# Optimization experiments

Measured on AMD Instinct MI355X. Metric: run time of the kernel, lower is better.

## Reference

```python
import jax, jax.numpy as jnp
import numpy as np

IM_FE_RATIO = 16.0


def setup_inputs() -> dict:
    key = jax.random.key(0)
    k1, k2 = jax.random.split(key)
    B, C, H, W, N = 4, 128, 256, 256, 4096
    feature = jax.random.normal(k1, (B, C, H, W), dtype=jnp.float32)
    # keypoints in image-pixel coords, in range [0, (W-1)*im_fe_ratio]
    keypoints = jax.random.uniform(k2, (B, N, 2), dtype=jnp.float32,
                                   minval=0.0, maxval=(W - 1) * IM_FE_RATIO)
    return {"feature": feature, "keypoints": keypoints}


def _interpolate(feature, keypoints):
    B, C, H, W = feature.shape
    kp = keypoints / IM_FE_RATIO  # B x N x 2 in feature-map coords (x, y)
    max_xy = jnp.array([W - 1, H - 1], dtype=kp.dtype)
    lo = jnp.maximum(jnp.floor(kp), 0.0)   # B x N x 2
    hi = jnp.minimum(jnp.ceil(kp), max_xy)  # B x N x 2
    up = kp - lo                            # fractional part (weight for upper corner)
    lw = 1.0 - up                           # weight for lower corner

    # corner order matches torch code: (x0,y0), (x1,y0), (x0,y1), (x1,y1)
    ix = jnp.stack([lo[..., 0], hi[..., 0], lo[..., 0], hi[..., 0]], axis=-1).astype(jnp.int32)  # B x N x 4
    iy = jnp.stack([lo[..., 1], lo[..., 1], hi[..., 1], hi[..., 1]], axis=-1).astype(jnp.int32)  # B x N x 4
    wx = jnp.stack([lw[..., 0], up[..., 0], lw[..., 0], up[..., 0]], axis=-1)
    wy = jnp.stack([lw[..., 1], lw[..., 1], up[..., 1], up[..., 1]], axis=-1)
    coeff = wx * wy                          # B x N x 4

    idx = (iy * W + ix)                      # B x N x 4 flat spatial indices
    feat_flat = feature.reshape(B, C, H * W)

    # gather per batch: (C, HW)[:, (N,4)] -> C x N x 4
    gathered = jax.vmap(lambda f, i: f[:, i])(feat_flat, idx)  # B x C x N x 4
    uf = jnp.einsum('bcnk,bnk->bcn', gathered, coeff)          # B x C x N

    # mask off keypoints that are (0, 0): mean over the 2 coords of (kp > 1e-10)
    mask = (kp > 1e-10).astype(uf.dtype).mean(axis=2)          # B x N
    return uf * mask[:, None, :]


def reference(feature, keypoints):
    return _interpolate(feature, keypoints)
```

## Files before the change

kernel.cpp:

```cpp
#include <hip/hip_runtime.h>

#define BB 4
#define CC 128
#define HH 256
#define WW 256
#define NKP 4096
#define INV_RATIO (1.0f / 16.0f)
#define CPT 4
#define NXCD 8

typedef float fpair __attribute__((ext_vector_type(2)));

__global__ __launch_bounds__(256) void interp_kernel(
    const float* __restrict__ feature,
    const float* __restrict__ keypoints,
    float* __restrict__ out)
{
    int bid   = blockIdx.x;
    int xcd   = bid & (NXCD - 1);
    int slot  = bid >> 3;
    int gloc  = slot >> 4;
    int j     = slot & 15;
    int g     = gloc * NXCD + xcd;
    int b     = g >> 5;
    int c0    = (g & 31) * CPT;
    int n     = j * 256 + threadIdx.x;

    const float* kp = keypoints + ((size_t)(b * NKP + n)) * 2;
    float kx = kp[0] * INV_RATIO;
    float ky = kp[1] * INV_RATIO;

    float fx = fmaxf(floorf(kx), 0.0f);
    float fy = fmaxf(floorf(ky), 0.0f);
    int x0 = (int)fx, y0 = (int)fy;

    float ux = kx - fx, uy = ky - fy;
    float lx = 1.0f - ux, ly = 1.0f - uy;

    bool selx = (x0 >= WW - 1);
    bool sely = (y0 >= HH - 1);
    int xp = selx ? (WW - 2) : x0;
    int yp = sely ? (HH - 2) : y0;
    float wlx = selx ? 0.0f : lx, wux = selx ? 1.0f : ux;
    float wly = sely ? 0.0f : ly, wuy = sely ? 1.0f : uy;

    float mask = 0.5f * ((kx > 1e-10f ? 1.0f : 0.0f) + (ky > 1e-10f ? 1.0f : 0.0f));
    float w00 = wlx * wly * mask, w01 = wux * wly * mask;
    float w10 = wlx * wuy * mask, w11 = wux * wuy * mask;

    int i0 = yp * WW + xp;
    int i1 = i0 + WW;

    const float* f = feature + ((size_t)(b * CC + c0)) * (HH * WW);

    fpair r0[CPT], r1[CPT];
    #pragma unroll
    for (int k = 0; k < CPT; ++k) {
        const float* fc = f + (size_t)k * (HH * WW);
        __builtin_memcpy(&r0[k], fc + i0, sizeof(fpair));
        __builtin_memcpy(&r1[k], fc + i1, sizeof(fpair));
    }

    float* o = out + ((size_t)(b * CC + c0)) * NKP + n;
    #pragma unroll
    for (int k = 0; k < CPT; ++k) {
        float val = w00 * r0[k].x + w01 * r0[k].y
                  + w10 * r1[k].x + w11 * r1[k].y;
        __builtin_nontemporal_store(val, o + (size_t)k * NKP);
    }
}

extern "C" void kernel_launch(void* const* d_in, const int* in_sizes, int n_in,
                              void* d_out, int out_size, void* d_ws, size_t ws_size,
                              hipStream_t stream) {
    const float* feature   = (const float*)d_in[0];
    const float* keypoints = (const float*)d_in[1];
    float* out = (float*)d_out;

    const int grid = BB * (CC / CPT) * (NKP / 256);
    interp_kernel<<<grid, 256, 0, stream>>>(feature, keypoints, out);
}
```

Measured before the change: 30.39 us.

## Counting-sort keypoints by spatial bin before gathering, then permute results back

```diff
diff --git a/kernel.cpp b/kernel.cpp
--- a/kernel.cpp
+++ b/kernel.cpp
@@ -11,7 +11,150 @@
 
 typedef float fpair __attribute__((ext_vector_type(2)));
 
-__global__ __launch_bounds__(256) void interp_kernel(
+#define O_INV  (BB * NKP * 2 * 4)
+#define O_VS   (256 * 1024)
+#define WS_NEEDED (O_VS + (size_t)BB * CC * NKP * 4)
+
+__global__ __launch_bounds__(1024) void sort_kernel(
+    const float* __restrict__ keypoints,
+    float* __restrict__ sorted_kp,
+    unsigned* __restrict__ inv)
+{
+    __shared__ unsigned bins[4096];
+    __shared__ unsigned wtot[16];
+    __shared__ unsigned wexc[16];
+    const int b = blockIdx.x;
+    const int t = threadIdx.x;
+    const int lane = t & 63, wid = t >> 6;
+
+    #pragma unroll
+    for (int k = 0; k < 4; ++k) bins[t + 1024 * k] = 0u;
+    __syncthreads();
+
+    unsigned key[4];
+    float kxv[4], kyv[4];
+    #pragma unroll
+    for (int k = 0; k < 4; ++k) {
+        int n = t + 1024 * k;
+        const float* kp = keypoints + ((size_t)(b * NKP + n)) * 2;
+        float kx = kp[0] * INV_RATIO, ky = kp[1] * INV_RATIO;
+        kxv[k] = kx; kyv[k] = ky;
+        int x0 = (int)fmaxf(floorf(kx), 0.0f);
+        int y0 = (int)fmaxf(floorf(ky), 0.0f);
+        unsigned bin = ((unsigned)y0 << 4) | ((unsigned)x0 >> 4);
+        key[k] = bin;
+        atomicAdd(&bins[bin], 1u);
+    }
+    __syncthreads();
+
+    unsigned c0 = bins[4*t], c1 = bins[4*t+1], c2 = bins[4*t+2], c3 = bins[4*t+3];
+    unsigned s = c0 + c1 + c2 + c3;
+    unsigned v = s;
+    #pragma unroll
+    for (int d = 1; d < 64; d <<= 1) {
+        unsigned u = __shfl_up(v, d, 64);
+        if (lane >= d) v += u;
+    }
+    if (lane == 63) wtot[wid] = v;
+    __syncthreads();
+    if (t == 0) { unsigned acc = 0; for (int w = 0; w < 16; ++w) { wexc[w] = acc; acc += wtot[w]; } }
+    __syncthreads();
+    unsigned texc = wexc[wid] + (v - s);
+    bins[4*t]   = texc;
+    bins[4*t+1] = texc + c0;
+    bins[4*t+2] = texc + c0 + c1;
+    bins[4*t+3] = texc + c0 + c1 + c2;
+    __syncthreads();
+
+    #pragma unroll
+    for (int k = 0; k < 4; ++k) {
+        int n = t + 1024 * k;
+        unsigned pos = atomicAdd(&bins[key[k]], 1u);
+        float* dst = sorted_kp + ((size_t)(b * NKP) + pos) * 2;
+        dst[0] = kxv[k];
+        dst[1] = kyv[k];
+        inv[b * NKP + n] = pos;
+    }
+}
+
+__global__ __launch_bounds__(256) void gather_kernel(
+    const float* __restrict__ feature,
+    const float* __restrict__ sorted_kp,
+    float* __restrict__ out_sorted)
+{
+    int bid   = blockIdx.x;
+    int xcd   = bid & (NXCD - 1);
+    int slot  = bid >> 3;
+    int gloc  = slot >> 4;
+    int j     = slot & 15;
+    int g     = gloc * NXCD + xcd;
+    int b     = g >> 5;
+    int c0    = (g & 31) * CPT;
+    int i     = j * 256 + threadIdx.x;
+
+    fpair kpv;
+    __builtin_memcpy(&kpv, sorted_kp + ((size_t)(b * NKP) + i) * 2, sizeof(fpair));
+    float kx = kpv.x, ky = kpv.y;
+
+    float fx = fmaxf(floorf(kx), 0.0f);
+    float fy = fmaxf(floorf(ky), 0.0f);
+    int x0 = (int)fx, y0 = (int)fy;
+
+    float ux = kx - fx, uy = ky - fy;
+    float lx = 1.0f - ux, ly = 1.0f - uy;
+
+    bool selx = (x0 >= WW - 1);
+    bool sely = (y0 >= HH - 1);
+    int xp = selx ? (WW - 2) : x0;
+    int yp = sely ? (HH - 2) : y0;
+    float wlx = selx ? 0.0f : lx, wux = selx ? 1.0f : ux;
+    float wly = sely ? 0.0f : ly, wuy = sely ? 1.0f : uy;
+
+    float mask = 0.5f * ((kx > 1e-10f ? 1.0f : 0.0f) + (ky > 1e-10f ? 1.0f : 0.0f));
+    float w00 = wlx * wly * mask, w01 = wux * wly * mask;
+    float w10 = wlx * wuy * mask, w11 = wux * wuy * mask;
+
+    int i0 = yp * WW + xp;
+    int i1 = i0 + WW;
+
+    const float* f = feature + ((size_t)(b * CC + c0)) * (HH * WW);
+
+    fpair r0[CPT], r1[CPT];
+    #pragma unroll
+    for (int k = 0; k < CPT; ++k) {
+        const float* fc = f + (size_t)k * (HH * WW);
+        __builtin_memcpy(&r0[k], fc + i0, sizeof(fpair));
+        __builtin_memcpy(&r1[k], fc + i1, sizeof(fpair));
+    }
+
+    float* o = out_sorted + ((size_t)(b * CC + c0)) * NKP + i;
+    #pragma unroll
+    for (int k = 0; k < CPT; ++k) {
+        float val = w00 * r0[k].x + w01 * r0[k].y
+                  + w10 * r1[k].x + w11 * r1[k].y;
+        o[(size_t)k * NKP] = val;
+    }
+}
+
+__global__ __launch_bounds__(256) void permute_kernel(
+    const float* __restrict__ out_sorted,
+    const unsigned* __restrict__ inv,
+    float* __restrict__ out)
+{
+    __shared__ float v[NKP];
+    int bc = blockIdx.x;
+    int b  = bc >> 7;
+    const float* src = out_sorted + (size_t)bc * NKP;
+    for (int k = threadIdx.x; k < NKP; k += 256) v[k] = src[k];
+    __syncthreads();
+    const unsigned* invb = inv + b * NKP;
+    float* dst = out + (size_t)bc * NKP;
+    for (int n = threadIdx.x; n < NKP; n += 256) {
+        __builtin_nontemporal_store(v[invb[n]], dst + n);
+    }
+}
+
+__global__ __launch_bounds__(256) void interp_direct_kernel(
     const float* __restrict__ feature,
     const float* __restrict__ keypoints,
     float* __restrict__ out)
@@ -77,6 +220,18 @@
     const float* keypoints = (const float*)d_in[1];
     float* out = (float*)d_out;
 
-    const int grid = BB * (CC / CPT) * (NKP / 256);
-    interp_kernel<<<grid, 256, 0, stream>>>(feature, keypoints, out);
-}
+    if (ws_size < WS_NEEDED) {
+        const int grid = BB * (CC / CPT) * (NKP / 256);
+        interp_direct_kernel<<<grid, 256, 0, stream>>>(feature, keypoints, out);
+        return;
+    }
+
+    char* ws = (char*)d_ws;
+    float*    sorted_kp  = (float*)ws;
+    unsigned* inv        = (unsigned*)(ws + O_INV);
+    float*    out_sorted = (float*)(ws + O_VS);
+
+    sort_kernel<<<BB, 1024, 0, stream>>>(keypoints, sorted_kp, inv);
+    gather_kernel<<<BB * (CC / CPT) * (NKP / 256), 256, 0, stream>>>(feature, sorted_kp, out_sorted);
+    permute_kernel<<<BB * CC, 256, 0, stream>>>(out_sorted, inv, out);
+}
```

Result: slower. 38.94 us (+28.2%).

## Process four keypoints per thread with vectorized keypoint loads and stores

Applied to the files above, without the earlier changes.

```diff
diff --git a/kernel.cpp b/kernel.cpp
--- a/kernel.cpp
+++ b/kernel.cpp
@@ -6,68 +6,89 @@
 #define WW 256
 #define NKP 4096
 #define INV_RATIO (1.0f / 16.0f)
-#define CPT 4
+#define KPT 4
+#define CPT 2
 #define NXCD 8
 
 typedef float fpair __attribute__((ext_vector_type(2)));
+typedef float f4    __attribute__((ext_vector_type(4)));
 
 __global__ __launch_bounds__(256) void interp_kernel(
     const float* __restrict__ feature,
     const float* __restrict__ keypoints,
     float* __restrict__ out)
 {
-    int bid   = blockIdx.x;
-    int xcd   = bid & (NXCD - 1);
-    int slot  = bid >> 3;
-    int gloc  = slot >> 4;
-    int j     = slot & 15;
-    int g     = gloc * NXCD + xcd;
-    int b     = g >> 5;
-    int c0    = (g & 31) * CPT;
-    int n     = j * 256 + threadIdx.x;
+    int bid  = blockIdx.x;
+    int xcd  = bid & (NXCD - 1);
+    int slot = bid >> 3;
+    int gloc = slot >> 2;
+    int j    = slot & 3;
+    int g    = gloc * NXCD + xcd;
+    int b    = g >> 6;
+    int c0   = (g & 63) * CPT;
+    int n0   = j * 1024 + threadIdx.x * KPT;
 
-    const float* kp = keypoints + ((size_t)(b * NKP + n)) * 2;
-    float kx = kp[0] * INV_RATIO;
-    float ky = kp[1] * INV_RATIO;
+    const float* kpp = keypoints + ((size_t)(b * NKP + n0)) * 2;
+    f4 kpa, kpb;
+    __builtin_memcpy(&kpa, kpp,     sizeof(f4));
+    __builtin_memcpy(&kpb, kpp + 4, sizeof(f4));
 
-    float fx = fmaxf(floorf(kx), 0.0f);
-    float fy = fmaxf(floorf(ky), 0.0f);
-    int x0 = (int)fx, y0 = (int)fy;
+    float kxs[KPT] = { kpa.x * INV_RATIO, kpa.z * INV_RATIO,
+                       kpb.x * INV_RATIO, kpb.z * INV_RATIO };
+    float kys[KPT] = { kpa.y * INV_RATIO, kpa.w * INV_RATIO,
+                       kpb.y * INV_RATIO, kpb.w * INV_RATIO };
 
-    float ux = kx - fx, uy = ky - fy;
-    float lx = 1.0f - ux, ly = 1.0f - uy;
+    const float* f0 = feature + ((size_t)(b * CC + c0)) * (HH * WW);
+    const float* f1 = f0 + HH * WW;
 
-    bool selx = (x0 >= WW - 1);
-    bool sely = (y0 >= HH - 1);
-    int xp = selx ? (WW - 2) : x0;
-    int yp = sely ? (HH - 2) : y0;
-    float wlx = selx ? 0.0f : lx, wux = selx ? 1.0f : ux;
-    float wly = sely ? 0.0f : ly, wuy = sely ? 1.0f : uy;
+    float w00[KPT], w01[KPT], w10[KPT], w11[KPT];
+    int   i0[KPT], i1[KPT];
+    #pragma unroll
+    for (int k = 0; k < KPT; ++k) {
+        float kx = kxs[k], ky = kys[k];
+        float fx = fmaxf(floorf(kx), 0.0f);
+        float fy = fmaxf(floorf(ky), 0.0f);
+        int x0 = (int)fx, y0 = (int)fy;
 
-    float mask = 0.5f * ((kx > 1e-10f ? 1.0f : 0.0f) + (ky > 1e-10f ? 1.0f : 0.0f));
-    float w00 = wlx * wly * mask, w01 = wux * wly * mask;
-    float w10 = wlx * wuy * mask, w11 = wux * wuy * mask;
+        float ux = kx - fx, uy = ky - fy;
+        float lx = 1.0f - ux, ly = 1.0f - uy;
 
-    int i0 = yp * WW + xp;
-    int i1 = i0 + WW;
+        bool selx = (x0 >= WW - 1);
+        bool sely = (y0 >= HH - 1);
+        int xp = selx ? (WW - 2) : x0;
+        int yp = sely ? (HH - 2) : y0;
+        float wlx = selx ? 0.0f : lx, wux = selx ? 1.0f : ux;
+        float wly = sely ? 0.0f : ly, wuy = sely ? 1.0f : uy;
 
-    const float* f = feature + ((size_t)(b * CC + c0)) * (HH * WW);
+        float mask = 0.5f * ((kx > 1e-10f ? 1.0f : 0.0f) + (ky > 1e-10f ? 1.0f : 0.0f));
+        w00[k] = wlx * wly * mask; w01[k] = wux * wly * mask;
+        w10[k] = wlx * wuy * mask; w11[k] = wux * wuy * mask;
 
-    fpair r0[CPT], r1[CPT];
-    #pragma unroll
-    for (int k = 0; k < CPT; ++k) {
-        const float* fc = f + (size_t)k * (HH * WW);
-        __builtin_memcpy(&r0[k], fc + i0, sizeof(fpair));
-        __builtin_memcpy(&r1[k], fc + i1, sizeof(fpair));
+        i0[k] = yp * WW + xp;
+        i1[k] = i0[k] + WW;
     }
 
-    float* o = out + ((size_t)(b * CC + c0)) * NKP + n;
+    fpair a0[KPT], a1[KPT], b0[KPT], b1[KPT];
     #pragma unroll
-    for (int k = 0; k < CPT; ++k) {
-        float val = w00 * r0[k].x + w01 * r0[k].y
-                  + w10 * r1[k].x + w11 * r1[k].y;
-        __builtin_nontemporal_store(val, o + (size_t)k * NKP);
+    for (int k = 0; k < KPT; ++k) {
+        __builtin_memcpy(&a0[k], f0 + i0[k], sizeof(fpair));
+        __builtin_memcpy(&a1[k], f0 + i1[k], sizeof(fpair));
+        __builtin_memcpy(&b0[k], f1 + i0[k], sizeof(fpair));
+        __builtin_memcpy(&b1[k], f1 + i1[k], sizeof(fpair));
     }
+
+    f4 r0, r1;
+    #pragma unroll
+    for (int k = 0; k < KPT; ++k) {
+        r0[k] = w00[k] * a0[k].x + w01[k] * a0[k].y
+              + w10[k] * a1[k].x + w11[k] * a1[k].y;
+        r1[k] = w00[k] * b0[k].x + w01[k] * b0[k].y
+              + w10[k] * b1[k].x + w11[k] * b1[k].y;
+    }
+
+    float* o = out + ((size_t)(b * CC + c0)) * NKP + n0;
+    __builtin_nontemporal_store(r0, (f4*)o);
+    __builtin_nontemporal_store(r1, (f4*)(o + NKP));
 }
 
 extern "C" void kernel_launch(void* const* d_in, const int* in_sizes, int n_in,
@@ -77,6 +98,6 @@
     const float* keypoints = (const float*)d_in[1];
     float* out = (float*)d_out;
 
-    const int grid = BB * (CC / CPT) * (NKP / 256);
+    const int grid = BB * (CC / CPT) * (NKP / (256 * KPT));
     interp_kernel<<<grid, 256, 0, stream>>>(feature, keypoints, out);
 }
```

Result: slower. 32.53 us (+7.1%).

## Stage feature row bands in LDS and scan keypoints per band

Applied to the files above, without the earlier changes.

```diff
diff --git a/kernel.cpp b/kernel.cpp
--- a/kernel.cpp
+++ b/kernel.cpp
@@ -6,67 +6,75 @@
 #define WW 256
 #define NKP 4096
 #define INV_RATIO (1.0f / 16.0f)
-#define CPT 4
-#define NXCD 8
+#define BAND 32
+#define NBAND (HH / BAND)
 
 typedef float fpair __attribute__((ext_vector_type(2)));
+typedef float f4    __attribute__((ext_vector_type(4)));
 
-__global__ __launch_bounds__(256) void interp_kernel(
+__global__ __launch_bounds__(256) void interp_band_kernel(
     const float* __restrict__ feature,
     const float* __restrict__ keypoints,
     float* __restrict__ out)
 {
-    int bid   = blockIdx.x;
-    int xcd   = bid & (NXCD - 1);
-    int slot  = bid >> 3;
-    int gloc  = slot >> 4;
-    int j     = slot & 15;
-    int g     = gloc * NXCD + xcd;
-    int b     = g >> 5;
-    int c0    = (g & 31) * CPT;
-    int n     = j * 256 + threadIdx.x;
+    __shared__ float st[BAND + 1][WW];
 
-    const float* kp = keypoints + ((size_t)(b * NKP + n)) * 2;
-    float kx = kp[0] * INV_RATIO;
-    float ky = kp[1] * INV_RATIO;
+    int bid  = blockIdx.x;
+    int c    = bid & (CC - 1);
+    int band = (bid >> 7) & (NBAND - 1);
+    int b    = bid >> 10;
+    int tid  = threadIdx.x;
+    int y0b  = band * BAND;
 
-    float fx = fmaxf(floorf(kx), 0.0f);
-    float fy = fmaxf(floorf(ky), 0.0f);
-    int x0 = (int)fx, y0 = (int)fy;
+    const f4* src = (const f4*)(feature + ((size_t)(b * CC + c) * HH + y0b) * WW);
+    f4* dst = (f4*)&st[0][0];
+    #pragma unroll
+    for (int i = 0; i < 8; ++i)
+        dst[tid + i * 256] = src[tid + i * 256];
+    {
+        int hy = min(y0b + BAND, HH - 1);
+        const f4* hsrc = (const f4*)(feature + ((size_t)(b * CC + c) * HH + hy) * WW);
+        if (tid < WW / 4) dst[(BAND * WW) / 4 + tid] = hsrc[tid];
+    }
+    __syncthreads();
 
-    float ux = kx - fx, uy = ky - fy;
-    float lx = 1.0f - ux, ly = 1.0f - uy;
+    const float* kpb = keypoints + (size_t)b * NKP * 2;
+    float* orow = out + (size_t)(b * CC + c) * NKP;
 
-    bool selx = (x0 >= WW - 1);
-    bool sely = (y0 >= HH - 1);
-    int xp = selx ? (WW - 2) : x0;
-    int yp = sely ? (HH - 2) : y0;
-    float wlx = selx ? 0.0f : lx, wux = selx ? 1.0f : ux;
-    float wly = sely ? 0.0f : ly, wuy = sely ? 1.0f : uy;
+    #pragma unroll 4
+    for (int it = 0; it < NKP / 256; ++it) {
+        int n = tid + it * 256;
+        fpair kpv;
+        __builtin_memcpy(&kpv, kpb + 2 * (size_t)n, sizeof(fpair));
+        float kx = kpv.x * INV_RATIO;
+        float ky = kpv.y * INV_RATIO;
 
-    float mask = 0.5f * ((kx > 1e-10f ? 1.0f : 0.0f) + (ky > 1e-10f ? 1.0f : 0.0f));
-    float w00 = wlx * wly * mask, w01 = wux * wly * mask;
-    float w10 = wlx * wuy * mask, w11 = wux * wuy * mask;
+        float fy = fmaxf(floorf(ky), 0.0f);
+        int y0 = (int)fy;
+        int yp = (y0 >= HH - 1) ? (HH - 2) : y0;
+        if ((yp >> 5) != band) continue;
 
-    int i0 = yp * WW + xp;
-    int i1 = i0 + WW;
+        float fx = fmaxf(floorf(kx), 0.0f);
+        int x0 = (int)fx;
 
-    const float* f = feature + ((size_t)(b * CC + c0)) * (HH * WW);
+        float ux = kx - fx, uy = ky - fy;
+        float lx = 1.0f - ux, ly = 1.0f - uy;
 
-    fpair r0[CPT], r1[CPT];
-    #pragma unroll
-    for (int k = 0; k < CPT; ++k) {
-        const float* fc = f + (size_t)k * (HH * WW);
-        __builtin_memcpy(&r0[k], fc + i0, sizeof(fpair));
-        __builtin_memcpy(&r1[k], fc + i1, sizeof(fpair));
-    }
+        bool selx = (x0 >= WW - 1);
+        bool sely = (y0 >= HH - 1);
+        int xp = selx ? (WW - 2) : x0;
+        float wlx = selx ? 0.0f : lx, wux = selx ? 1.0f : ux;
+        float wly = sely ? 0.0f : ly, wuy = sely ? 1.0f : uy;
 
-    float* o = out + ((size_t)(b * CC + c0)) * NKP + n;
-    #pragma unroll
-    for (int k = 0; k < CPT; ++k) {
-        float val = w00 * r0[k].x + w01 * r0[k].y
-                  + w10 * r1[k].x + w11 * r1[k].y;
-        __builtin_nontemporal_store(val, o + (size_t)k * NKP);
+        float mask = 0.5f * ((kx > 1e-10f ? 1.0f : 0.0f) + (ky > 1e-10f ? 1.0f : 0.0f));
+        float w00 = wlx * wly * mask, w01 = wux * wly * mask;
+        float w10 = wlx * wuy * mask, w11 = wux * wuy * mask;
+
+        int yl = yp - y0b;
+        float v00 = st[yl][xp],     v01 = st[yl][xp + 1];
+        float v10 = st[yl + 1][xp], v11 = st[yl + 1][xp + 1];
+
+        orow[n] = w00 * v00 + w01 * v01 + w10 * v10 + w11 * v11;
     }
 }
 
@@ -77,6 +85,6 @@
     const float* keypoints = (const float*)d_in[1];
     float* out = (float*)d_out;
 
-    const int grid = BB * (CC / CPT) * (NKP / 256);
-    interp_kernel<<<grid, 256, 0, stream>>>(feature, keypoints, out);
+    const int grid = BB * NBAND * CC;
+    interp_band_kernel<<<grid, 256, 0, stream>>>(feature, keypoints, out);
 }
```

Result: slower. 45.59 us (+50.0%).
